# Kernel tuning notes

Hardware: AMD Instinct MI355X
Metric: run time of the kernel (lower is better)

Reference implementation:

```python
import jax, jax.numpy as jnp
from jax import lax
import numpy as np

B, T, D, U, K = 32, 1000, 512, 5, 3  # batch, frames, idim, upsample_times, conv kernel (l_order+r_order+1)
THRESHOLD = 1.0
TAIL = 0.45


def setup_inputs() -> dict:
    key = jax.random.key(0)
    ks = jax.random.split(key, 6)
    return {
        "encoder_out": jax.random.normal(ks[0], (B, T, D), jnp.float32),
        "mask": jnp.ones((B, 1, T), jnp.float32),
        "conv_w": jax.random.normal(ks[1], (D, D, K), jnp.float32) * 0.02,  # torch Conv1d [out,in,k]
        "conv_b": jnp.zeros((D,), jnp.float32),
        "up_w": jax.random.normal(ks[2], (D, D, U), jnp.float32) * 0.02,    # torch ConvTranspose1d [in,out,k]
        "up_b": jnp.zeros((D,), jnp.float32),
        "w1": jax.random.normal(ks[3], (D,), jnp.float32) * 0.05,           # cif_output Linear(D,1)
        "b1": jnp.zeros((), jnp.float32),
        "w2": jax.random.normal(ks[4], (D,), jnp.float32) * 0.05,           # cif_output2 Linear(D,1)
        "b2": jnp.zeros((), jnp.float32),
    }


def _cif(hidden, alphas, threshold):
    # hidden: [B, Tt, D], alphas: [B, Tt]
    Bb, Tt, Dd = hidden.shape

    def step(carry, inp):
        integrate, frame = carry
        alpha, h_t = inp  # [B], [B, D]
        dist_completion = 1.0 - integrate
        integrate = integrate + alpha
        fires_t = integrate
        fire = integrate >= threshold
        integrate = jnp.where(fire, integrate - 1.0, integrate)
        cur = jnp.where(fire, dist_completion, alpha)
        frame_out = frame + cur[:, None] * h_t
        frame = jnp.where(fire[:, None], (alpha - cur)[:, None] * h_t, frame_out)
        return (integrate, frame), (fires_t, frame_out)

    init = (jnp.zeros((Bb,), hidden.dtype), jnp.zeros((Bb, Dd), hidden.dtype))
    _, (fires, frames) = lax.scan(step, init, (alphas.T, jnp.swapaxes(hidden, 0, 1)))
    fires = fires.T                      # [B, Tt]
    frames = jnp.swapaxes(frames, 0, 1)  # [B, Tt, D]

    fire_mask = fires >= threshold

    def gather_b(frames_b, mask_b):
        pos = jnp.cumsum(mask_b.astype(jnp.int32)) - 1
        pos = jnp.where(mask_b, pos, Tt)  # non-fires -> out of range, dropped
        return jnp.zeros((Tt, Dd), frames_b.dtype).at[pos].set(frames_b, mode='drop')

    acoustic = jax.vmap(gather_b)(frames, fire_mask)  # [B, Tt, D] zero-padded
    return acoustic, fires


def reference(encoder_out, mask, conv_w, conv_b, up_w, up_b, w1, b1, w2, b2):
    Bb, Tt, Dd = encoder_out.shape
    context = jnp.swapaxes(encoder_out, 1, 2)           # [B, D, T]
    queries = jnp.pad(context, ((0, 0), (0, 0), (1, 1)))  # ConstantPad1d((1,1))
    conv = lax.conv_general_dilated(queries, conv_w, (1,), 'VALID',
                                    dimension_numbers=('NCH', 'OIH', 'NCH'))
    output = jax.nn.relu(conv + conv_b[None, :, None])  # [B, D, T]

    # ConvTranspose1d(stride=kernel=U, pad=0): non-overlapping -> einsum
    out2 = jnp.einsum('bit,ioj->btjo', output, up_w).reshape(Bb, Tt * U, Dd) + up_b  # [B, T*U, D]
    alphas2 = jax.nn.relu(jax.nn.sigmoid(out2 @ w2 + b2) * 1.0 - 0.0)  # smooth_factor2=1, noise_threshold2=0
    mask2 = jnp.swapaxes(jnp.broadcast_to(mask, (Bb, U, Tt)), 1, 2).reshape(Bb, Tt * U)
    alphas2 = alphas2 * mask2
    token_num2 = alphas2.sum(-1)

    h1 = jnp.swapaxes(output, 1, 2)  # [B, T, D]
    alphas = jax.nn.relu(jax.nn.sigmoid(h1 @ w1 + b1) * 1.0 - 0.0)  # smooth_factor=1, noise_threshold=0
    maskT = jnp.swapaxes(mask, 1, 2)[..., 0]  # [B, T]
    alphas = alphas * maskT

    # tail_process_fn (tail_threshold=0.45, mask given)
    zeros_t = jnp.zeros((Bb, 1), alphas.dtype)
    ones_t = jnp.ones((Bb, 1), alphas.dtype)
    mask_1 = jnp.concatenate([maskT, zeros_t], axis=1)
    mask_2 = jnp.concatenate([ones_t, maskT], axis=1)
    tail_add = (mask_2 - mask_1) * TAIL
    alphas_t = jnp.concatenate([alphas, zeros_t], axis=1) + tail_add  # [B, T+1]
    hidden = jnp.concatenate([encoder_out, jnp.zeros((Bb, 1, Dd), encoder_out.dtype)], axis=1)
    token_num = jnp.floor(alphas_t.sum(-1))

    acoustic_embeds, cif_peak = _cif(hidden, alphas_t, THRESHOLD)
    return acoustic_embeds, token_num, alphas_t, cif_peak, token_num2
```

## Files before the change

kernel.cpp:

```cpp
#include <hip/hip_runtime.h>
#include <math.h>

#define TB 32
#define TT 1000
#define TD 512
#define TU 5
#define TT1 1001

#define OFF_ACC  0
#define OFF_TOKN 16400384
#define OFF_ALPH 16400416
#define OFF_PEAK 16432448
#define OFF_TOK2 16464480

typedef _Float16 half8 __attribute__((ext_vector_type(8)));
typedef _Float16 half2t __attribute__((ext_vector_type(2)));
typedef float float4t __attribute__((ext_vector_type(4)));

typedef __attribute__((address_space(3))) uint32_t lds_u32_t;
typedef __attribute__((address_space(1))) const uint32_t g_u32_t;
#define GLOAD_LDS(gp, lp) __builtin_amdgcn_global_load_lds((g_u32_t*)(gp), (lds_u32_t*)(lp), 16, 0, 0)

#define BSTR 72
#define ASTR 200
#define EROWS 1032

#define WS_ARAW1 0
#define WS_ARAW2 32000
#define WS_VMAT  192000
#define WS_C2    194560
#define WS_WA    194564
#define WS_WB    226596
#define WS_FIRE  258628
#define WS_NF    290660
#define WS_ENCS_BYTES 1163264ull
#define WS_CWS_BYTES  (WS_ENCS_BYTES + 76059648ull)
#define WS_NEED_BYTES (WS_CWS_BYTES + 3276800ull)

__global__ __launch_bounds__(256) void kzero(float* araw1, float* araw2, float* tok2) {
    int idx = blockIdx.x * 256 + threadIdx.x;
    int stride = gridDim.x * 256;
    for (int i = idx; i < TB * TT; i += stride) araw1[i] = 0.f;
    for (int i = idx; i < TB * TT * TU; i += stride) araw2[i] = 0.f;
    if (idx < TB) tok2[idx] = 0.f;
}

__global__ __launch_bounds__(256) void kc2(const float* __restrict__ up_b, const float* __restrict__ w2,
                                           const float* __restrict__ b2, float* __restrict__ c2out) {
    int tid = threadIdx.x;
    float p = 0.f;
    for (int o = tid; o < TD; o += 256) p += up_b[o] * w2[o];
#pragma unroll
    for (int m = 1; m < 64; m <<= 1) p += __shfl_xor(p, m);
    __shared__ float wsum[4];
    if ((tid & 63) == 0) wsum[tid >> 6] = p;
    __syncthreads();
    if (tid == 0) c2out[0] = b2[0] + wsum[0] + wsum[1] + wsum[2] + wsum[3];
}

__global__ __launch_bounds__(64) void kv(const float* __restrict__ up_w, const float* __restrict__ w2,
                                         float* __restrict__ vmat) {
    int i = blockIdx.x, lane = threadIdx.x;
    float s0 = 0, s1 = 0, s2 = 0, s3 = 0, s4 = 0;
    for (int o = lane; o < TD; o += 64) {
        float w = w2[o];
        const float* p = up_w + (size_t)i * (TD * TU) + o * TU;
        s0 += p[0] * w; s1 += p[1] * w; s2 += p[2] * w; s3 += p[3] * w; s4 += p[4] * w;
    }
#pragma unroll
    for (int m = 1; m < 64; m <<= 1) {
        s0 += __shfl_xor(s0, m); s1 += __shfl_xor(s1, m); s2 += __shfl_xor(s2, m);
        s3 += __shfl_xor(s3, m); s4 += __shfl_xor(s4, m);
    }
    if (lane == 0) {
        float* d = vmat + i * TU;
        d[0] = s0; d[1] = s1; d[2] = s2; d[3] = s3; d[4] = s4;
    }
}

__global__ __launch_bounds__(256) void ksplitE(const float* __restrict__ enc, _Float16* __restrict__ encs) {
    int t = blockIdx.x, b = blockIdx.y, tid = threadIdx.x;
    int c = tid * 2;
    const float* p = &enc[((size_t)b * TT + t) * TD + c];
    float x0 = p[0], x1 = p[1];
    _Float16 h0 = (_Float16)x0, h1 = (_Float16)x1;
    _Float16 l0 = (_Float16)(x0 - (float)h0), l1 = (_Float16)(x1 - (float)h1);
    int ic = c >> 5, pos = c & 31;
    size_t base = ((size_t)(b * 16 + ic) * EROWS + 1 + t) * BSTR + pos;
    encs[base] = h0; encs[base + 1] = h1;
    encs[base + 32] = l0; encs[base + 33] = l1;
}

__global__ __launch_bounds__(256) void kpad(_Float16* __restrict__ encs) {
    uint32_t* p = (uint32_t*)encs;
    int idx = blockIdx.x * 256 + threadIdx.x;
    int stride = gridDim.x * 256;
    const int total = 512 * 32 * 36;
    for (int u = idx; u < total; u += stride) {
        int bic = u / (32 * 36);
        int r = (u / 36) % 32;
        int w = u % 36;
        int row = (r == 0) ? 0 : 1000 + r;
        p[((size_t)bic * EROWS + row) * 36 + w] = 0u;
    }
}

__global__ __launch_bounds__(64) void ksplitW(const float* __restrict__ cw, _Float16* __restrict__ cws) {
    int o = blockIdx.x, lane = threadIdx.x;
    for (int u = lane; u < 16 * 32 * 3; u += 64) {
        int tap = u % 3, pos = (u / 3) % 32, ic = u / 96;
        float x = cw[((size_t)o * TD + ic * 32 + pos) * 3 + tap];
        _Float16 h = (_Float16)x;
        _Float16 l = (_Float16)(x - (float)h);
        size_t base = (((size_t)(o >> 5) * 16 + ic) * 32 + (o & 31)) * ASTR + tap * 64;
        cws[base + pos] = h;
        cws[base + 32 + pos] = l;
    }
}

__global__ __launch_bounds__(256, 3) void kconvMD(const _Float16* __restrict__ encs,
                                                  const _Float16* __restrict__ cws,
                                                  const float* __restrict__ cb, const float* __restrict__ w1,
                                                  const float* __restrict__ vmat,
                                                  float* __restrict__ araw1, float* __restrict__ araw2) {
    __shared__ _Float16 sB[258 * BSTR];
    __shared__ _Float16 sA[32 * ASTR];

    const int tid = threadIdx.x;
    const int t0 = blockIdx.x * 256;
    const int oc = blockIdx.y;
    const int b = blockIdx.z;
    const int o0 = oc * 32;
    const int wv = tid >> 6, lane = tid & 63;
    const int q = lane >> 4, l15 = lane & 15;

    float4t acc[2][4];
#pragma unroll
    for (int i = 0; i < 2; ++i)
#pragma unroll
        for (int j = 0; j < 4; ++j) acc[i][j] = (float4t){0.f, 0.f, 0.f, 0.f};

    for (int ic = 0; ic < 16; ++ic) {
        __syncthreads();
        const _Float16* gB = encs + ((size_t)(b * 16 + ic) * EROWS + t0) * BSTR;
        for (int c = tid; c < 2322; c += 256) GLOAD_LDS(gB + c * 8, &sB[c * 8]);
        const _Float16* gA = cws + ((size_t)(oc * 16 + ic) * 32) * ASTR;
        for (int c = tid; c < 800; c += 256) GLOAD_LDS(gA + c * 8, &sA[c * 8]);
        __syncthreads();
#pragma unroll
        for (int tap = 0; tap < 3; ++tap) {
            half8 Bh[4], Bl[4];
#pragma unroll
            for (int tt = 0; tt < 4; ++tt) {
                int s = wv * 64 + tt * 16 + l15 + tap;
                Bh[tt] = *(const half8*)&sB[s * BSTR + q * 8];
                Bl[tt] = *(const half8*)&sB[s * BSTR + 32 + q * 8];
            }
#pragma unroll
            for (int ot = 0; ot < 2; ++ot) {
                const int orow = ot * 16 + l15;
                half8 Ah = *(const half8*)&sA[orow * ASTR + tap * 64 + q * 8];
                half8 Al = *(const half8*)&sA[orow * ASTR + tap * 64 + 32 + q * 8];
#pragma unroll
                for (int tt = 0; tt < 4; ++tt) {
                    acc[ot][tt] = __builtin_amdgcn_mfma_f32_16x16x32_f16(Ah, Bh[tt], acc[ot][tt], 0, 0, 0);
                    acc[ot][tt] = __builtin_amdgcn_mfma_f32_16x16x32_f16(Ah, Bl[tt], acc[ot][tt], 0, 0, 0);
                    acc[ot][tt] = __builtin_amdgcn_mfma_f32_16x16x32_f16(Al, Bh[tt], acc[ot][tt], 0, 0, 0);
                }
            }
        }
    }

#pragma unroll
    for (int tt = 0; tt < 4; ++tt) {
        int t = t0 + wv * 64 + tt * 16 + l15;
        float s1 = 0.f, sa = 0.f, sb = 0.f, sc = 0.f, sd = 0.f, se = 0.f;
#pragma unroll
        for (int ot = 0; ot < 2; ++ot) {
#pragma unroll
            for (int r = 0; r < 4; ++r) {
                int o = o0 + ot * 16 + q * 4 + r;
                float rv = fmaxf(acc[ot][tt][r] + cb[o], 0.f);
                s1 = fmaf(w1[o], rv, s1);
                const float* vp = &vmat[o * 5];
                sa = fmaf(vp[0], rv, sa); sb = fmaf(vp[1], rv, sb);
                sc = fmaf(vp[2], rv, sc); sd = fmaf(vp[3], rv, sd);
                se = fmaf(vp[4], rv, se);
            }
        }
        s1 += __shfl_xor(s1, 16); sa += __shfl_xor(sa, 16); sb += __shfl_xor(sb, 16);
        sc += __shfl_xor(sc, 16); sd += __shfl_xor(sd, 16); se += __shfl_xor(se, 16);
        s1 += __shfl_xor(s1, 32); sa += __shfl_xor(sa, 32); sb += __shfl_xor(sb, 32);
        sc += __shfl_xor(sc, 32); sd += __shfl_xor(sd, 32); se += __shfl_xor(se, 32);
        if (q == 0 && t < TT) {
            atomicAdd(&araw1[b * TT + t], s1);
            float* p2 = &araw2[(b * TT + t) * 5];
            atomicAdd(p2 + 0, sa); atomicAdd(p2 + 1, sb); atomicAdd(p2 + 2, sc);
            atomicAdd(p2 + 3, sd); atomicAdd(p2 + 4, se);
        }
    }
}

__global__ __launch_bounds__(256, 3) void kconvM(const float* __restrict__ enc, const float* __restrict__ cw,
                                                 const float* __restrict__ cb, const float* __restrict__ w1,
                                                 const float* __restrict__ vmat,
                                                 float* __restrict__ araw1, float* __restrict__ araw2) {
    __shared__ _Float16 sB[258 * BSTR];
    __shared__ _Float16 sA[32 * ASTR];

    const int tid = threadIdx.x;
    const int t0 = blockIdx.x * 256;
    const int o0 = blockIdx.y * 32;
    const int b = blockIdx.z;
    const int wv = tid >> 6, lane = tid & 63;
    const int q = lane >> 4, l15 = lane & 15;

    float4t acc[2][4];
#pragma unroll
    for (int i = 0; i < 2; ++i)
#pragma unroll
        for (int j = 0; j < 4; ++j) acc[i][j] = (float4t){0.f, 0.f, 0.f, 0.f};

    for (int i0 = 0; i0 < TD; i0 += 32) {
        __syncthreads();
        for (int u = tid; u < 258 * 16; u += 256) {
            int s = u >> 4, ii2 = (u & 15) << 1;
            int t = t0 - 1 + s;
            float x0 = 0.f, x1 = 0.f;
            if (t >= 0 && t < TT) {
                const float* p = &enc[((size_t)b * TT + t) * TD + i0 + ii2];
                x0 = p[0]; x1 = p[1];
            }
            _Float16 h0 = (_Float16)x0, h1 = (_Float16)x1;
            _Float16 l0 = (_Float16)(x0 - (float)h0), l1 = (_Float16)(x1 - (float)h1);
            half2t hh; hh[0] = h0; hh[1] = h1;
            half2t ll; ll[0] = l0; ll[1] = l1;
            *(half2t*)&sB[s * BSTR + ii2] = hh;
            *(half2t*)&sB[s * BSTR + 32 + ii2] = ll;
        }
        for (int u = tid; u < 32 * 16; u += 256) {
            int o = u >> 4, ii2 = (u & 15) << 1;
            const float* p = &cw[((size_t)(o0 + o) * TD + i0 + ii2) * 3];
#pragma unroll
            for (int k = 0; k < 3; ++k) {
                float x0 = p[k], x1 = p[3 + k];
                _Float16 h0 = (_Float16)x0, h1 = (_Float16)x1;
                _Float16 l0 = (_Float16)(x0 - (float)h0), l1 = (_Float16)(x1 - (float)h1);
                half2t hh; hh[0] = h0; hh[1] = h1;
                half2t ll; ll[0] = l0; ll[1] = l1;
                *(half2t*)&sA[o * ASTR + k * 64 + ii2] = hh;
                *(half2t*)&sA[o * ASTR + k * 64 + 32 + ii2] = ll;
            }
        }
        __syncthreads();
#pragma unroll
        for (int tap = 0; tap < 3; ++tap) {
            half8 Bh[4], Bl[4];
#pragma unroll
            for (int tt = 0; tt < 4; ++tt) {
                int s = wv * 64 + tt * 16 + l15 + tap;
                Bh[tt] = *(const half8*)&sB[s * BSTR + q * 8];
                Bl[tt] = *(const half8*)&sB[s * BSTR + 32 + q * 8];
            }
#pragma unroll
            for (int ot = 0; ot < 2; ++ot) {
                const int orow = ot * 16 + l15;
                half8 Ah = *(const half8*)&sA[orow * ASTR + tap * 64 + q * 8];
                half8 Al = *(const half8*)&sA[orow * ASTR + tap * 64 + 32 + q * 8];
#pragma unroll
                for (int tt = 0; tt < 4; ++tt) {
                    acc[ot][tt] = __builtin_amdgcn_mfma_f32_16x16x32_f16(Ah, Bh[tt], acc[ot][tt], 0, 0, 0);
                    acc[ot][tt] = __builtin_amdgcn_mfma_f32_16x16x32_f16(Ah, Bl[tt], acc[ot][tt], 0, 0, 0);
                    acc[ot][tt] = __builtin_amdgcn_mfma_f32_16x16x32_f16(Al, Bh[tt], acc[ot][tt], 0, 0, 0);
                }
            }
        }
    }

#pragma unroll
    for (int tt = 0; tt < 4; ++tt) {
        int t = t0 + wv * 64 + tt * 16 + l15;
        float s1 = 0.f, sa = 0.f, sb = 0.f, sc = 0.f, sd = 0.f, se = 0.f;
#pragma unroll
        for (int ot = 0; ot < 2; ++ot) {
#pragma unroll
            for (int r = 0; r < 4; ++r) {
                int o = o0 + ot * 16 + q * 4 + r;
                float rv = fmaxf(acc[ot][tt][r] + cb[o], 0.f);
                s1 = fmaf(w1[o], rv, s1);
                const float* vp = &vmat[o * 5];
                sa = fmaf(vp[0], rv, sa); sb = fmaf(vp[1], rv, sb);
                sc = fmaf(vp[2], rv, sc); sd = fmaf(vp[3], rv, sd);
                se = fmaf(vp[4], rv, se);
            }
        }
        s1 += __shfl_xor(s1, 16); sa += __shfl_xor(sa, 16); sb += __shfl_xor(sb, 16);
        sc += __shfl_xor(sc, 16); sd += __shfl_xor(sd, 16); se += __shfl_xor(se, 16);
        s1 += __shfl_xor(s1, 32); sa += __shfl_xor(sa, 32); sb += __shfl_xor(sb, 32);
        sc += __shfl_xor(sc, 32); sd += __shfl_xor(sd, 32); se += __shfl_xor(se, 32);
        if (q == 0 && t < TT) {
            atomicAdd(&araw1[b * TT + t], s1);
            float* p2 = &araw2[(b * TT + t) * 5];
            atomicAdd(p2 + 0, sa); atomicAdd(p2 + 1, sb); atomicAdd(p2 + 2, sc);
            atomicAdd(p2 + 3, sd); atomicAdd(p2 + 4, se);
        }
    }
}

__global__ __launch_bounds__(256) void kalpha(const float* __restrict__ araw1, const float* __restrict__ araw2,
                                              const float* __restrict__ mask, const float* __restrict__ b1,
                                              const float* __restrict__ c2,
                                              float* __restrict__ alphas_t, float* __restrict__ tok2) {
    int b = blockIdx.y;
    int t = blockIdx.x * 256 + threadIdx.x;
    float sum5 = 0.f;
    if (t < TT) {
        float mk = mask[b * TT + t];
        float a1 = araw1[b * TT + t] + b1[0];
        float alpha = mk / (1.f + expf(-a1));
        float mprev = (t == 0) ? 1.f : mask[b * TT + t - 1];
        float tail = (mprev - mk) * 0.45f;
        alphas_t[b * TT1 + t] = alpha + tail;
        float cc = c2[0];
        float x0 = araw2[(b * TT + t) * 5 + 0] + cc;
        float x1 = araw2[(b * TT + t) * 5 + 1] + cc;
        float x2 = araw2[(b * TT + t) * 5 + 2] + cc;
        float x3 = araw2[(b * TT + t) * 5 + 3] + cc;
        float x4 = araw2[(b * TT + t) * 5 + 4] + cc;
        sum5 = mk / (1.f + expf(-x0)) + mk / (1.f + expf(-x1)) + mk / (1.f + expf(-x2))
             + mk / (1.f + expf(-x3)) + mk / (1.f + expf(-x4));
    } else if (t == TT) {
        alphas_t[b * TT1 + TT] = mask[b * TT + TT - 1] * 0.45f;
    }
#pragma unroll
    for (int m = 1; m < 64; m <<= 1) sum5 += __shfl_xor(sum5, m);
    if ((threadIdx.x & 63) == 0) atomicAdd(&tok2[b], sum5);
}

#define STEP(j, aj) { \
    float dist = 1.f - integ; \
    integ += (aj); \
    sp[tq + (j)] = integ; \
    bool fire = integ >= 1.f; \
    float cur = fire ? dist : (aj); \
    swa[tq + (j)] = cur; \
    swb[tq + (j)] = fire ? ((aj) - cur) : 0.f; \
    if (fire) { sf[F++] = tq + (j); integ -= 1.f; } \
    Ssum += (aj); }

__global__ __launch_bounds__(64) void kscan(const float* __restrict__ alphas_t,
                                            float* __restrict__ cif_peak, float* __restrict__ token_num,
                                            float* __restrict__ wA, float* __restrict__ wB,
                                            int* __restrict__ fire_time, int* __restrict__ n_fires) {
    __shared__ float sa[TT1 + 7], sp[TT1], swa[TT1], swb[TT1];
    __shared__ int sf[TT1];
    __shared__ int sFs;
    int b = blockIdx.x, lane = threadIdx.x;
    for (int t = lane; t < TT1 + 7; t += 64) sa[t] = (t < TT1) ? alphas_t[b * TT1 + t] : 0.f;
    __syncthreads();
    if (lane == 0) {
        float integ = 0.f, Ssum = 0.f;
        int F = 0;
        for (int tq = 0; tq < TT1 - 1; tq += 8) {
            float a0 = sa[tq], a1 = sa[tq + 1], a2 = sa[tq + 2], a3 = sa[tq + 3];
            float a4 = sa[tq + 4], a5 = sa[tq + 5], a6 = sa[tq + 6], a7 = sa[tq + 7];
            STEP(0, a0) STEP(1, a1) STEP(2, a2) STEP(3, a3)
            STEP(4, a4) STEP(5, a5) STEP(6, a6) STEP(7, a7)
        }
        { int tq = TT1 - 1; float a0 = sa[tq]; STEP(0, a0) }
        token_num[b] = floorf(Ssum);
        n_fires[b] = F;
        sFs = F;
    }
    __syncthreads();
    int F = sFs;
    for (int t = lane; t < TT1; t += 64) {
        cif_peak[b * TT1 + t] = sp[t];
        wA[b * TT1 + t] = swa[t];
        wB[b * TT1 + t] = swb[t];
        if (t < F) fire_time[b * TT1 + t] = sf[t];
    }
}

__global__ __launch_bounds__(128) void kgather(const float* __restrict__ enc,
                                               const float* __restrict__ wA, const float* __restrict__ wB,
                                               const int* __restrict__ fire_time, const int* __restrict__ n_fires,
                                               float* __restrict__ acoustic) {
    int k = blockIdx.x, b = blockIdx.y;
    int d4 = threadIdx.x;
    float ox = 0.f, oy = 0.f, oz = 0.f, ow = 0.f;
    int nf = n_fires[b];
    if (k < nf) {
        int end = fire_time[b * TT1 + k];
        int start = (k > 0) ? fire_time[b * TT1 + k - 1] : 0;
        for (int t = start; t <= end; ++t) {
            if (t >= TT) continue;
            float w = (k > 0 && t == start) ? wB[b * TT1 + t] : wA[b * TT1 + t];
            float4 h = ((const float4*)(enc + ((size_t)b * TT + t) * TD))[d4];
            ox += w * h.x; oy += w * h.y; oz += w * h.z; ow += w * h.w;
        }
    }
    float4 o4; o4.x = ox; o4.y = oy; o4.z = oz; o4.w = ow;
    ((float4*)(acoustic + ((size_t)b * TT1 + k) * TD))[d4] = o4;
}

extern "C" void kernel_launch(void* const* d_in, const int* in_sizes, int n_in,
                              void* d_out, int out_size, void* d_ws, size_t ws_size,
                              hipStream_t stream) {
    (void)in_sizes; (void)n_in; (void)out_size;
    const float* enc = (const float*)d_in[0];
    const float* mask = (const float*)d_in[1];
    const float* cw = (const float*)d_in[2];
    const float* cb = (const float*)d_in[3];
    const float* upw = (const float*)d_in[4];
    const float* upb = (const float*)d_in[5];
    const float* w1 = (const float*)d_in[6];
    const float* b1 = (const float*)d_in[7];
    const float* w2 = (const float*)d_in[8];
    const float* b2 = (const float*)d_in[9];

    float* out = (float*)d_out;
    float* acoustic = out + OFF_ACC;
    float* token_num = out + OFF_TOKN;
    float* alphas_t = out + OFF_ALPH;
    float* cif_peak = out + OFF_PEAK;
    float* tok2 = out + OFF_TOK2;

    float* ws = (float*)d_ws;
    float* araw1 = ws + WS_ARAW1;
    float* araw2 = ws + WS_ARAW2;
    float* vmat = ws + WS_VMAT;
    float* c2 = ws + WS_C2;
    float* wA = ws + WS_WA;
    float* wB = ws + WS_WB;
    int* fire_time = (int*)(ws + WS_FIRE);
    int* n_fires = (int*)(ws + WS_NF);
    _Float16* encs = (_Float16*)((char*)d_ws + WS_ENCS_BYTES);
    _Float16* cws = (_Float16*)((char*)d_ws + WS_CWS_BYTES);

    const bool bigws = (ws_size >= WS_NEED_BYTES);

    hipLaunchKernelGGL(kzero, dim3(256), dim3(256), 0, stream, araw1, araw2, tok2);
    hipLaunchKernelGGL(kc2, dim3(1), dim3(256), 0, stream, upb, w2, b2, c2);
    hipLaunchKernelGGL(kv, dim3(TD), dim3(64), 0, stream, upw, w2, vmat);
    if (bigws) {
        hipLaunchKernelGGL(kpad, dim3(1024), dim3(256), 0, stream, encs);
        hipLaunchKernelGGL(ksplitE, dim3(TT, TB), dim3(256), 0, stream, enc, encs);
        hipLaunchKernelGGL(ksplitW, dim3(TD), dim3(64), 0, stream, cw, cws);
        hipLaunchKernelGGL(kconvMD, dim3(4, 16, TB), dim3(256), 0, stream, encs, cws, cb, w1, vmat, araw1, araw2);
    } else {
        hipLaunchKernelGGL(kconvM, dim3(4, 16, TB), dim3(256), 0, stream, enc, cw, cb, w1, vmat, araw1, araw2);
    }
    hipLaunchKernelGGL(kalpha, dim3(4, TB), dim3(256), 0, stream, araw1, araw2, mask, b1, c2, alphas_t, tok2);
    hipLaunchKernelGGL(kscan, dim3(TB), dim3(64), 0, stream, alphas_t, cif_peak, token_num, wA, wB, fire_time, n_fires);
    hipLaunchKernelGGL(kgather, dim3(TT1, TB), dim3(128), 0, stream, enc, wA, wB, fire_time, n_fires, acoustic);
}
```

Before: 409.3 us.

## Widen conv tile to 128 output channels per block to reuse encoder tile

Each conv block now computes 128 output channels instead of 32, loading four weight slices into dynamic shared memory per input-channel chunk. The same encoder tile in LDS is reused four times as often, cutting repeated global and LDS traffic for the activations by a factor of four. In exchange, accumulator registers grow fourfold, occupancy drops to one block per CU, the grid shrinks fourfold, and the MFMA loop order is rearranged. Launching needs a one-time dynamic shared-memory attribute.

```diff
diff --git a/kernel.cpp b/kernel.cpp
--- a/kernel.cpp
+++ b/kernel.cpp
@@ -24,6 +24,9 @@
 #define BSTR 72
 #define ASTR 200
 #define EROWS 1032
+
+#define SB_HALVES 18576
+#define SMEM_BYTES ((SB_HALVES + 128 * ASTR) * 2)
 
 #define WS_ARAW1 0
 #define WS_ARAW2 32000
@@ -118,34 +121,39 @@
     }
 }
 
-__global__ __launch_bounds__(256, 3) void kconvMD(const _Float16* __restrict__ encs,
+__global__ __launch_bounds__(256, 1) void kconvMD(const _Float16* __restrict__ encs,
                                                   const _Float16* __restrict__ cws,
                                                   const float* __restrict__ cb, const float* __restrict__ w1,
                                                   const float* __restrict__ vmat,
                                                   float* __restrict__ araw1, float* __restrict__ araw2) {
-    __shared__ _Float16 sB[258 * BSTR];
-    __shared__ _Float16 sA[32 * ASTR];
+    extern __shared__ _Float16 smem[];
+    _Float16* sB = smem;
+    _Float16* sA = smem + SB_HALVES;
 
     const int tid = threadIdx.x;
     const int t0 = blockIdx.x * 256;
-    const int oc = blockIdx.y;
+    const int oc4 = blockIdx.y * 4;
     const int b = blockIdx.z;
-    const int o0 = oc * 32;
+    const int o0 = blockIdx.y * 128;
     const int wv = tid >> 6, lane = tid & 63;
     const int q = lane >> 4, l15 = lane & 15;
 
-    float4t acc[2][4];
-#pragma unroll
-    for (int i = 0; i < 2; ++i)
+    float4t acc[8][4];
+#pragma unroll
+    for (int i = 0; i < 8; ++i)
 #pragma unroll
         for (int j = 0; j < 4; ++j) acc[i][j] = (float4t){0.f, 0.f, 0.f, 0.f};
 
+#pragma unroll 1
     for (int ic = 0; ic < 16; ++ic) {
         __syncthreads();
         const _Float16* gB = encs + ((size_t)(b * 16 + ic) * EROWS + t0) * BSTR;
         for (int c = tid; c < 2322; c += 256) GLOAD_LDS(gB + c * 8, &sB[c * 8]);
-        const _Float16* gA = cws + ((size_t)(oc * 16 + ic) * 32) * ASTR;
-        for (int c = tid; c < 800; c += 256) GLOAD_LDS(gA + c * 8, &sA[c * 8]);
+#pragma unroll
+        for (int g = 0; g < 4; ++g) {
+            const _Float16* gA = cws + ((size_t)((oc4 + g) * 16 + ic) * 32) * ASTR;
+            for (int c = tid; c < 800; c += 256) GLOAD_LDS(gA + c * 8, &sA[g * 6400 + c * 8]);
+        }
         __syncthreads();
 #pragma unroll
         for (int tap = 0; tap < 3; ++tap) {
@@ -157,16 +165,19 @@
                 Bl[tt] = *(const half8*)&sB[s * BSTR + 32 + q * 8];
             }
 #pragma unroll
-            for (int ot = 0; ot < 2; ++ot) {
+            for (int ot = 0; ot < 8; ++ot) {
                 const int orow = ot * 16 + l15;
                 half8 Ah = *(const half8*)&sA[orow * ASTR + tap * 64 + q * 8];
                 half8 Al = *(const half8*)&sA[orow * ASTR + tap * 64 + 32 + q * 8];
 #pragma unroll
-                for (int tt = 0; tt < 4; ++tt) {
+                for (int tt = 0; tt < 4; ++tt)
                     acc[ot][tt] = __builtin_amdgcn_mfma_f32_16x16x32_f16(Ah, Bh[tt], acc[ot][tt], 0, 0, 0);
+#pragma unroll
+                for (int tt = 0; tt < 4; ++tt)
                     acc[ot][tt] = __builtin_amdgcn_mfma_f32_16x16x32_f16(Ah, Bl[tt], acc[ot][tt], 0, 0, 0);
+#pragma unroll
+                for (int tt = 0; tt < 4; ++tt)
                     acc[ot][tt] = __builtin_amdgcn_mfma_f32_16x16x32_f16(Al, Bh[tt], acc[ot][tt], 0, 0, 0);
-                }
             }
         }
     }
@@ -176,7 +187,7 @@
         int t = t0 + wv * 64 + tt * 16 + l15;
         float s1 = 0.f, sa = 0.f, sb = 0.f, sc = 0.f, sd = 0.f, se = 0.f;
 #pragma unroll
-        for (int ot = 0; ot < 2; ++ot) {
+        for (int ot = 0; ot < 8; ++ot) {
 #pragma unroll
             for (int r = 0; r < 4; ++r) {
                 int o = o0 + ot * 16 + q * 4 + r;
@@ -440,6 +451,13 @@
 
     const bool bigws = (ws_size >= WS_NEED_BYTES);
 
+    static bool attr_set = false;
+    if (!attr_set) {
+        hipFuncSetAttribute(reinterpret_cast<const void*>(&kconvMD),
+                            hipFuncAttributeMaxDynamicSharedMemorySize, SMEM_BYTES);
+        attr_set = true;
+    }
+
     hipLaunchKernelGGL(kzero, dim3(256), dim3(256), 0, stream, araw1, araw2, tok2);
     hipLaunchKernelGGL(kc2, dim3(1), dim3(256), 0, stream, upb, w2, b2, c2);
     hipLaunchKernelGGL(kv, dim3(TD), dim3(64), 0, stream, upw, w2, vmat);
@@ -447,7 +465,8 @@
         hipLaunchKernelGGL(kpad, dim3(1024), dim3(256), 0, stream, encs);
         hipLaunchKernelGGL(ksplitE, dim3(TT, TB), dim3(256), 0, stream, enc, encs);
         hipLaunchKernelGGL(ksplitW, dim3(TD), dim3(64), 0, stream, cw, cws);
-        hipLaunchKernelGGL(kconvMD, dim3(4, 16, TB), dim3(256), 0, stream, encs, cws, cb, w1, vmat, araw1, araw2);
+        hipLaunchKernelGGL(kconvMD, dim3(4, 4, TB), dim3(256), SMEM_BYTES, stream,
+                           encs, cws, cb, w1, vmat, araw1, araw2);
     } else {
         hipLaunchKernelGGL(kconvM, dim3(4, 16, TB), dim3(256), 0, stream, enc, cw, cb, w1, vmat, araw1, araw2);
     }
```

New measurement: 415.7 us. Within noise of the previous version (+1.6%).
